# Kernel optimization log

Measured on AMD Instinct MI355X. Metric: run time of the kernel, lower is better.

The kernel has to match this reference:

```python
import jax, jax.numpy as jnp
import numpy as np

TOP_K = 2


def setup_inputs() -> dict:
    key = jax.random.key(0)
    k1, k2, k3, k4, k5 = jax.random.split(key, 5)
    B, S, H, F, E = 4, 2048, 1024, 4096, 8
    scale = 1.0 / np.sqrt(H)
    return {
        "hidden_states": jax.random.normal(k1, (B, S, H), dtype=jnp.float32),
        "gate_w": jax.random.normal(k2, (E, H), dtype=jnp.float32) * scale,
        "w1": jax.random.normal(k3, (E, F, H), dtype=jnp.float32) * scale,
        "w3": jax.random.normal(k4, (E, F, H), dtype=jnp.float32) * scale,
        "w2": jax.random.normal(k5, (E, H, F), dtype=jnp.float32) * (1.0 / np.sqrt(F)),
    }


def reference(hidden_states, gate_w, w1, w3, w2):
    B, S, H = hidden_states.shape
    E = gate_w.shape[0]
    x = hidden_states.reshape(-1, H)                    # [T, H], T = B*S

    router_logits = x @ gate_w.T                        # [T, E]
    probs = jax.nn.softmax(router_logits.astype(jnp.float32), axis=-1)
    top_w, top_i = jax.lax.top_k(probs, TOP_K)          # [T, k]
    top_w = top_w / jnp.sum(top_w, axis=-1, keepdims=True)
    top_w = top_w.astype(x.dtype)

    # combine weight of each expert for each token: [E, T]
    one_hot = jax.nn.one_hot(top_i, E, dtype=x.dtype)   # [T, k, E]
    comb = jnp.einsum("tke,tk->et", one_hot, top_w)

    # loop over experts via scan; tokens not routed to expert e have comb==0,
    # which matches the gather/FFN/scatter-combine of the original exactly.
    def body(acc, wts):
        w1e, w3e, w2e, ce = wts
        h = jax.nn.silu(x @ w1e.T) * (x @ w3e.T)        # [T, F]
        return acc + (h @ w2e.T) * ce[:, None], None

    out0 = jnp.zeros_like(x)
    out, _ = jax.lax.scan(body, out0, (w1, w3, w2, comb))
    return out.reshape(B, S, H), router_logits
```

## Files before the change

kernel.cpp:

```cpp
#include <hip/hip_runtime.h>
#include <hip/hip_bf16.h>

#define T_TOK 8192
#define HDIM  1024
#define FDIM  4096
#define NEXP  8
#define CVT_BLKS 2048

typedef __attribute__((ext_vector_type(8))) short short8;
typedef __attribute__((ext_vector_type(4))) float f32x4;
typedef unsigned short u16;
typedef unsigned int   u32;

#define XB_OFF    0ull
#define W1B_OFF   (XB_OFF   + 16777216ull)
#define W3B_OFF   (W1B_OFF  + 67108864ull)
#define W2B_OFF   (W3B_OFF  + 67108864ull)
#define HBUF_OFF  (W2B_OFF  + 67108864ull)
#define CNT_OFF   (HBUF_OFF + 134217728ull)
#define HOFF_OFF  (CNT_OFF  + 64ull)
#define TLIST_OFF (HOFF_OFF + 64ull)
#define WLIST_OFF (TLIST_OFF + 262144ull)
#define WS_NEED   (WLIST_OFF + 262144ull)

__device__ __forceinline__ u16 f2bf(float f) {
  u32 u = __float_as_uint(f);
  return (u16)((u + 0x7fffu + ((u >> 16) & 1u)) >> 16);
}
__device__ __forceinline__ float bf2f(u16 v) {
  return __uint_as_float((u32)v << 16);
}

__device__ __forceinline__ void gl_lds16(const void* g, void* l) {
  __builtin_amdgcn_global_load_lds(
      (const __attribute__((address_space(1))) void*)g,
      (__attribute__((address_space(3))) void*)l, 16, 0, 0);
}

__global__ __launch_bounds__(256) void prep_kernel(
    const float* __restrict__ x, const float* __restrict__ gw,
    const float* __restrict__ s0, const float* __restrict__ s1,
    u16* __restrict__ d0, u16* __restrict__ d1,
    float* __restrict__ logits, u16* __restrict__ xb,
    int* __restrict__ counts, int* __restrict__ tlist,
    float* __restrict__ wt1, float* __restrict__ wt2,
    int* __restrict__ slot1, int* __restrict__ slot2) {
  if (blockIdx.x < 8192) {
    const int n8 = NEXP * FDIM * HDIM / 8;
    const int total = 2 * n8;
    const int stride = 8192 * 256;
    for (int i = blockIdx.x * 256 + threadIdx.x; i < total; i += stride) {
      int seg = i >> 22;
      int j = i & (n8 - 1);
      const float* s = seg == 0 ? s0 : s1;
      u16* d = seg == 0 ? d0 : d1;
      float4 v0 = ((const float4*)s)[j * 2];
      float4 v1 = ((const float4*)s)[j * 2 + 1];
      uint4 o;
      o.x = (u32)f2bf(v0.x) | ((u32)f2bf(v0.y) << 16);
      o.y = (u32)f2bf(v0.z) | ((u32)f2bf(v0.w) << 16);
      o.z = (u32)f2bf(v1.x) | ((u32)f2bf(v1.y) << 16);
      o.w = (u32)f2bf(v1.z) | ((u32)f2bf(v1.w) << 16);
      ((uint4*)d)[j] = o;
    }
    return;
  }
  const int wid = threadIdx.x >> 6, lane = threadIdx.x & 63;
  const int t = (blockIdx.x - 8192) * 4 + wid;
  const float* xr = x + (size_t)t * HDIM + lane * 16;
  float4 xv[4];
#pragma unroll
  for (int q = 0; q < 4; ++q) xv[q] = ((const float4*)xr)[q];

  u32 pk[8];
#pragma unroll
  for (int q = 0; q < 4; ++q) {
    pk[q * 2 + 0] = (u32)f2bf(xv[q].x) | ((u32)f2bf(xv[q].y) << 16);
    pk[q * 2 + 1] = (u32)f2bf(xv[q].z) | ((u32)f2bf(xv[q].w) << 16);
  }
  u32* xbo = (u32*)(xb + (size_t)t * HDIM + lane * 16);
  ((uint4*)xbo)[0] = make_uint4(pk[0], pk[1], pk[2], pk[3]);
  ((uint4*)xbo)[1] = make_uint4(pk[4], pk[5], pk[6], pk[7]);

  float lg[NEXP];
#pragma unroll
  for (int e = 0; e < NEXP; ++e) {
    const float4* g = (const float4*)(gw + (size_t)e * HDIM + lane * 16);
    float s = 0.f;
#pragma unroll
    for (int q = 0; q < 4; ++q) {
      float4 gv = g[q];
      s += xv[q].x * gv.x + xv[q].y * gv.y + xv[q].z * gv.z + xv[q].w * gv.w;
    }
#pragma unroll
    for (int off = 32; off > 0; off >>= 1) s += __shfl_xor(s, off, 64);
    lg[e] = s;
  }
  if (lane == 0) {
    float* lo = logits + (size_t)t * NEXP;
#pragma unroll
    for (int e = 0; e < NEXP; ++e) lo[e] = lg[e];
    float v1 = -1e30f, v2 = -1e30f; int i1 = 0, i2 = 0;
#pragma unroll
    for (int e = 0; e < NEXP; ++e) {
      float le = lg[e];
      if (le > v1)      { v2 = v1; i2 = i1; v1 = le; i1 = e; }
      else if (le > v2) { v2 = le; i2 = e; }
    }
    float t2 = __expf(v2 - v1);
    float rs = 1.f / (1.f + t2);
    int p1 = atomicAdd(&counts[i1], 1);
    tlist[i1 * T_TOK + p1] = t;
    slot1[t] = (i1 << 16) | p1;  wt1[t] = rs;
    int p2 = atomicAdd(&counts[i2], 1);
    tlist[i2 * T_TOK + p2] = t;
    slot2[t] = (i2 << 16) | p2;  wt2[t] = t2 * rs;
  }
}

__global__ void prefix_kernel(const int* __restrict__ counts, int* __restrict__ hoff) {
  if (threadIdx.x == 0) {
    int s = 0;
    for (int e = 0; e < NEXP; ++e) { hoff[e] = s; s += counts[e]; }
    hoff[NEXP] = s;
  }
}

__global__ __launch_bounds__(256, 4) void ffn1_kernel(
    const u16* __restrict__ xb, const u16* __restrict__ w1b, const u16* __restrict__ w3b,
    u16* __restrict__ hbuf, const int* __restrict__ counts, const int* __restrict__ hoff,
    const int* __restrict__ tlist,
    const float* __restrict__ w2src, u16* __restrict__ w2b) {
  if (blockIdx.x < CVT_BLKS) {
    const int n8 = NEXP * HDIM * FDIM / 8;
    const int stride = CVT_BLKS * 256;
    for (int j = blockIdx.x * 256 + threadIdx.x; j < n8; j += stride) {
      float4 v0 = ((const float4*)w2src)[j * 2];
      float4 v1 = ((const float4*)w2src)[j * 2 + 1];
      uint4 o;
      o.x = (u32)f2bf(v0.x) | ((u32)f2bf(v0.y) << 16);
      o.y = (u32)f2bf(v0.z) | ((u32)f2bf(v0.w) << 16);
      o.z = (u32)f2bf(v1.x) | ((u32)f2bf(v1.y) << 16);
      o.w = (u32)f2bf(v1.z) | ((u32)f2bf(v1.w) << 16);
      ((uint4*)w2b)[j] = o;
    }
    return;
  }
  const int bid = blockIdx.x - CVT_BLKS;
  const int e  = bid & 7;
  const int j  = bid >> 3;
  const int ct = j >> 6;
  const int rt = j & 63;
  const int Ne = counts[e];
  if (rt * 128 >= Ne) return;

  __shared__ u16 LDS[16384];

  const int tid = threadIdx.x;
  const int wid = tid >> 6, lane = tid & 63;
  const int wr = wid >> 1, wc = wid & 1;
  const int lr = lane & 15, lhi = lane >> 4;

  size_t aoff[4];
#pragma unroll
  for (int q = 0; q < 4; ++q) {
    int idx = q * 256 + tid;
    int r = idx >> 3, c = idx & 7;
    int grow = rt * 128 + r;
    int gi = grow < Ne ? grow : Ne - 1;
    aoff[q] = (size_t)tlist[e * T_TOK + gi] * HDIM + (size_t)((c ^ (r & 7)) * 8);
  }
  size_t boff[2];
#pragma unroll
  for (int q = 0; q < 2; ++q) {
    int idx = q * 256 + tid;
    int r = idx >> 3, c = idx & 7;
    boff[q] = ((size_t)e * FDIM + ct * 64 + r) * HDIM + (size_t)((c ^ (r & 7)) * 8);
  }
  const int dW = wid * 64 * 8;

  f32x4 acc1[4][2] = {}, acc3[4][2] = {};

  for (int k0 = 0; k0 < HDIM; k0 += 64) {
    __syncthreads();
#pragma unroll
    for (int q = 0; q < 4; ++q)
      gl_lds16(xb + aoff[q] + k0, LDS + q * 2048 + dW);
#pragma unroll
    for (int q = 0; q < 2; ++q) {
      gl_lds16(w1b + boff[q] + k0, LDS + 8192 + q * 2048 + dW);
      gl_lds16(w3b + boff[q] + k0, LDS + 12288 + q * 2048 + dW);
    }
    __syncthreads();
#pragma unroll
    for (int kk = 0; kk < 2; ++kk) {
      const int chn = ((kk * 4 + lhi) ^ (lr & 7)) * 8;
      short8 af[4], b1f[2], b3f[2];
#pragma unroll
      for (int m = 0; m < 4; ++m)
        af[m] = *(const short8*)(LDS + (wr * 64 + m * 16 + lr) * 64 + chn);
#pragma unroll
      for (int n = 0; n < 2; ++n) {
        int ro = (wc * 32 + n * 16 + lr) * 64 + chn;
        b1f[n] = *(const short8*)(LDS + 8192 + ro);
        b3f[n] = *(const short8*)(LDS + 12288 + ro);
      }
#pragma unroll
      for (int m = 0; m < 4; ++m)
#pragma unroll
        for (int n = 0; n < 2; ++n) {
          acc1[m][n] = __builtin_amdgcn_mfma_f32_16x16x32_bf16(af[m], b1f[n], acc1[m][n], 0, 0, 0);
          acc3[m][n] = __builtin_amdgcn_mfma_f32_16x16x32_bf16(af[m], b3f[n], acc3[m][n], 0, 0, 0);
        }
    }
  }

  const int hb = hoff[e];
  const int rbase = rt * 128 + wr * 64 + lhi * 4;
  const int cbase = ct * 64 + wc * 32 + lr;
#pragma unroll
  for (int m = 0; m < 4; ++m)
#pragma unroll
    for (int i = 0; i < 4; ++i) {
      int grow = rbase + m * 16 + i;
      if (grow < Ne) {
        size_t rowp = (size_t)(hb + grow) * FDIM + cbase;
#pragma unroll
        for (int n = 0; n < 2; ++n) {
          float a1 = acc1[m][n][i], a3 = acc3[m][n][i];
          hbuf[rowp + n * 16] = f2bf((a1 / (1.f + __expf(-a1))) * a3);
        }
      }
    }
}

__global__ __launch_bounds__(256, 4) void ffn2_kernel(
    const u16* __restrict__ hbuf, const u16* __restrict__ w2b,
    u16* __restrict__ ybuf, const int* __restrict__ counts, const int* __restrict__ hoff) {
  const int bid = blockIdx.x;
  const int e  = bid & 7;
  const int j  = bid >> 3;
  const int ct = j >> 6;
  const int rt = j & 63;
  const int Ne = counts[e];
  if (rt * 128 >= Ne) return;
  const int hb = hoff[e];

  __shared__ u16 Alds[128 * 64];
  __shared__ u16 Blds[128 * 64];

  const int tid = threadIdx.x;
  const int wid = tid >> 6, lane = tid & 63;
  const int wr = wid >> 1, wc = wid & 1;
  const int lr = lane & 15, lhi = lane >> 4;

  size_t aoff[4], boff[4]; int ldso[4];
#pragma unroll
  for (int q = 0; q < 4; ++q) {
    int i = wid * 4 + q;
    int r = i * 8 + (lane >> 3);
    int sw = ((lane & 7) ^ (r & 7)) * 8;
    int grow = rt * 128 + r;
    int gi = grow < Ne ? grow : Ne - 1;
    aoff[q] = (size_t)(hb + gi) * FDIM + sw;
    int hr = ct * 128 + r;
    boff[q] = ((size_t)e * HDIM + hr) * FDIM + sw;
    ldso[q] = i * 512;
  }

  f32x4 acc[4][4] = {};

  for (int k0 = 0; k0 < FDIM; k0 += 64) {
    __syncthreads();
#pragma unroll
    for (int q = 0; q < 4; ++q) {
      gl_lds16(hbuf + aoff[q] + k0, Alds + ldso[q]);
      gl_lds16(w2b + boff[q] + k0, Blds + ldso[q]);
    }
    __syncthreads();
#pragma unroll
    for (int kk = 0; kk < 2; ++kk) {
      const int swo = ((kk * 4 + lhi) ^ (lr & 7)) * 8;
      short8 af[4], bf_[4];
#pragma unroll
      for (int m = 0; m < 4; ++m)
        af[m] = *(const short8*)(Alds + (wr * 64 + m * 16 + lr) * 64 + swo);
#pragma unroll
      for (int n = 0; n < 4; ++n)
        bf_[n] = *(const short8*)(Blds + (wc * 64 + n * 16 + lr) * 64 + swo);
#pragma unroll
      for (int m = 0; m < 4; ++m)
#pragma unroll
        for (int n = 0; n < 4; ++n)
          acc[m][n] = __builtin_amdgcn_mfma_f32_16x16x32_bf16(af[m], bf_[n], acc[m][n], 0, 0, 0);
    }
  }

  const int rb = rt * 128 + wr * 64 + lhi * 4;
  const int cb = ct * 128 + wc * 64 + lr;
#pragma unroll
  for (int m = 0; m < 4; ++m)
#pragma unroll
    for (int i = 0; i < 4; ++i) {
      int grow = rb + m * 16 + i;
      if (grow < Ne) {
        u16* yp = ybuf + (size_t)(hb + grow) * HDIM + cb;
#pragma unroll
        for (int n = 0; n < 4; ++n)
          yp[n * 16] = f2bf(acc[m][n][i]);
      }
    }
}

__global__ __launch_bounds__(256) void combine_kernel(
    const u16* __restrict__ ybuf, const int* __restrict__ slot1, const int* __restrict__ slot2,
    const float* __restrict__ wt1, const float* __restrict__ wt2,
    const int* __restrict__ hoff, float* __restrict__ out) {
  int idx = blockIdx.x * 256 + threadIdx.x;
  int t = idx >> 7, c8 = (idx & 127) * 8;
  int s1 = slot1[t], s2 = slot2[t];
  float w1 = wt1[t], w2 = wt2[t];
  size_t r1 = (size_t)(hoff[s1 >> 16] + (s1 & 0xFFFF)) * HDIM + c8;
  size_t r2 = (size_t)(hoff[s2 >> 16] + (s2 & 0xFFFF)) * HDIM + c8;
  short8 y1 = *(const short8*)(ybuf + r1);
  short8 y2 = *(const short8*)(ybuf + r2);
  float* op = out + (size_t)t * HDIM + c8;
#pragma unroll
  for (int k = 0; k < 8; ++k)
    op[k] = w1 * bf2f((u16)y1[k]) + w2 * bf2f((u16)y2[k]);
}

extern "C" void kernel_launch(void* const* d_in, const int* in_sizes, int n_in,
                              void* d_out, int out_size, void* d_ws, size_t ws_size,
                              hipStream_t stream) {
  (void)in_sizes; (void)n_in; (void)out_size;
  if (ws_size < WS_NEED) return;

  const float* x  = (const float*)d_in[0];
  const float* gw = (const float*)d_in[1];
  const float* w1 = (const float*)d_in[2];
  const float* w3 = (const float*)d_in[3];
  const float* w2 = (const float*)d_in[4];
  float* out = (float*)d_out;
  float* logits = out + (size_t)T_TOK * HDIM;

  char* ws = (char*)d_ws;
  u16* xb    = (u16*)(ws + XB_OFF);
  u16* w1b   = (u16*)(ws + W1B_OFF);
  u16* w3b   = (u16*)(ws + W3B_OFF);
  u16* w2b   = (u16*)(ws + W2B_OFF);
  u16* hbuf  = (u16*)(ws + HBUF_OFF);
  u16* ybuf  = (u16*)(ws + W1B_OFF);
  int* counts = (int*)(ws + CNT_OFF);
  int* hoffp  = (int*)(ws + HOFF_OFF);
  int* tlist  = (int*)(ws + TLIST_OFF);
  float* wt1  = (float*)(ws + WLIST_OFF);
  float* wt2  = wt1 + T_TOK;
  int* slot1  = (int*)(wt2 + T_TOK);
  int* slot2  = slot1 + T_TOK;

  hipMemsetAsync(counts, 0, NEXP * sizeof(int), stream);

  prep_kernel<<<8192 + 2048, 256, 0, stream>>>(x, gw, w1, w3, w1b, w3b,
                                               logits, xb, counts, tlist,
                                               wt1, wt2, slot1, slot2);
  prefix_kernel<<<1, 64, 0, stream>>>(counts, hoffp);
  ffn1_kernel<<<CVT_BLKS + NEXP * 64 * 64, 256, 0, stream>>>(
      xb, w1b, w3b, hbuf, counts, hoffp, tlist, w2, w2b);
  ffn2_kernel<<<NEXP * 64 * 8, 256, 0, stream>>>(hbuf, w2b, ybuf, counts, hoffp);
  combine_kernel<<<T_TOK * 128 / 256, 256, 0, stream>>>(ybuf, slot1, slot2, wt1, wt2, hoffp, out);
}
```

Baseline: 780.8 us.

## Switch expert GEMMs to 32x32x16 MFMA and inline prefix offsets

Both expert FFN GEMM kernels now use 32x32x16 bf16 MFMA tiles instead of 16x16x32. This halves the number of LDS fragment reads per MFMA and cuts instruction count, with the epilogue rewritten for the 32x32 accumulator layout. The separate single-thread prefix kernel is removed: each block computes its expert row offset from counts directly, which saves a tiny launch at the cost of a few redundant loads per block. The larger accumulator vectors may raise register pressure under the 4-blocks launch bound.

```diff
diff --git a/kernel.cpp b/kernel.cpp
--- a/kernel.cpp
+++ b/kernel.cpp
@@ -7,8 +7,8 @@
 #define NEXP  8
 #define CVT_BLKS 2048
 
-typedef __attribute__((ext_vector_type(8))) short short8;
-typedef __attribute__((ext_vector_type(4))) float f32x4;
+typedef __attribute__((ext_vector_type(8)))  short short8;
+typedef __attribute__((ext_vector_type(16))) float f32x16;
 typedef unsigned short u16;
 typedef unsigned int   u32;
 
@@ -18,8 +18,7 @@
 #define W2B_OFF   (W3B_OFF  + 67108864ull)
 #define HBUF_OFF  (W2B_OFF  + 67108864ull)
 #define CNT_OFF   (HBUF_OFF + 134217728ull)
-#define HOFF_OFF  (CNT_OFF  + 64ull)
-#define TLIST_OFF (HOFF_OFF + 64ull)
+#define TLIST_OFF (CNT_OFF  + 128ull)
 #define WLIST_OFF (TLIST_OFF + 262144ull)
 #define WS_NEED   (WLIST_OFF + 262144ull)
 
@@ -118,18 +117,9 @@
   }
 }
 
-__global__ void prefix_kernel(const int* __restrict__ counts, int* __restrict__ hoff) {
-  if (threadIdx.x == 0) {
-    int s = 0;
-    for (int e = 0; e < NEXP; ++e) { hoff[e] = s; s += counts[e]; }
-    hoff[NEXP] = s;
-  }
-}
-
 __global__ __launch_bounds__(256, 4) void ffn1_kernel(
     const u16* __restrict__ xb, const u16* __restrict__ w1b, const u16* __restrict__ w3b,
-    u16* __restrict__ hbuf, const int* __restrict__ counts, const int* __restrict__ hoff,
-    const int* __restrict__ tlist,
+    u16* __restrict__ hbuf, const int* __restrict__ counts, const int* __restrict__ tlist,
     const float* __restrict__ w2src, u16* __restrict__ w2b) {
   if (blockIdx.x < CVT_BLKS) {
     const int n8 = NEXP * HDIM * FDIM / 8;
@@ -153,13 +143,16 @@
   const int rt = j & 63;
   const int Ne = counts[e];
   if (rt * 128 >= Ne) return;
+  int hb = 0;
+#pragma unroll
+  for (int i = 0; i < NEXP; ++i) hb += (i < e) ? counts[i] : 0;
 
   __shared__ u16 LDS[16384];
 
   const int tid = threadIdx.x;
   const int wid = tid >> 6, lane = tid & 63;
   const int wr = wid >> 1, wc = wid & 1;
-  const int lr = lane & 15, lhi = lane >> 4;
+  const int l31 = lane & 31, l5 = lane >> 5;
 
   size_t aoff[4];
 #pragma unroll
@@ -177,9 +170,11 @@
     int r = idx >> 3, c = idx & 7;
     boff[q] = ((size_t)e * FDIM + ct * 64 + r) * HDIM + (size_t)((c ^ (r & 7)) * 8);
   }
-  const int dW = wid * 64 * 8;
-
-  f32x4 acc1[4][2] = {}, acc3[4][2] = {};
+  const int dW = wid * 512;
+
+  const int rowA0 = wr * 64 + l31;
+  const int rowB  = wc * 32 + l31;
+  f32x16 acc1[2] = {{0}}, acc3[2] = {{0}};
 
   for (int k0 = 0; k0 < HDIM; k0 += 64) {
     __syncthreads();
@@ -193,50 +188,41 @@
     }
     __syncthreads();
 #pragma unroll
-    for (int kk = 0; kk < 2; ++kk) {
-      const int chn = ((kk * 4 + lhi) ^ (lr & 7)) * 8;
-      short8 af[4], b1f[2], b3f[2];
-#pragma unroll
-      for (int m = 0; m < 4; ++m)
-        af[m] = *(const short8*)(LDS + (wr * 64 + m * 16 + lr) * 64 + chn);
-#pragma unroll
-      for (int n = 0; n < 2; ++n) {
-        int ro = (wc * 32 + n * 16 + lr) * 64 + chn;
-        b1f[n] = *(const short8*)(LDS + 8192 + ro);
-        b3f[n] = *(const short8*)(LDS + 12288 + ro);
-      }
-#pragma unroll
-      for (int m = 0; m < 4; ++m)
-#pragma unroll
-        for (int n = 0; n < 2; ++n) {
-          acc1[m][n] = __builtin_amdgcn_mfma_f32_16x16x32_bf16(af[m], b1f[n], acc1[m][n], 0, 0, 0);
-          acc3[m][n] = __builtin_amdgcn_mfma_f32_16x16x32_bf16(af[m], b3f[n], acc3[m][n], 0, 0, 0);
-        }
-    }
-  }
-
-  const int hb = hoff[e];
-  const int rbase = rt * 128 + wr * 64 + lhi * 4;
-  const int cbase = ct * 64 + wc * 32 + lr;
-#pragma unroll
-  for (int m = 0; m < 4; ++m)
-#pragma unroll
-    for (int i = 0; i < 4; ++i) {
-      int grow = rbase + m * 16 + i;
+    for (int kk = 0; kk < 4; ++kk) {
+      const int cbase = kk * 2 + l5;
+      short8 af[2], b1v, b3v;
+#pragma unroll
+      for (int m = 0; m < 2; ++m) {
+        int r = rowA0 + m * 32;
+        af[m] = *(const short8*)(LDS + r * 64 + ((cbase ^ (r & 7)) * 8));
+      }
+      b1v = *(const short8*)(LDS + 8192  + rowB * 64 + ((cbase ^ (rowB & 7)) * 8));
+      b3v = *(const short8*)(LDS + 12288 + rowB * 64 + ((cbase ^ (rowB & 7)) * 8));
+#pragma unroll
+      for (int m = 0; m < 2; ++m) {
+        acc1[m] = __builtin_amdgcn_mfma_f32_32x32x16_bf16(af[m], b1v, acc1[m], 0, 0, 0);
+        acc3[m] = __builtin_amdgcn_mfma_f32_32x32x16_bf16(af[m], b3v, acc3[m], 0, 0, 0);
+      }
+    }
+  }
+
+  const int rbase = rt * 128 + wr * 64;
+  const int cbase = ct * 64 + wc * 32 + l31;
+#pragma unroll
+  for (int m = 0; m < 2; ++m)
+#pragma unroll
+    for (int r16 = 0; r16 < 16; ++r16) {
+      int grow = rbase + m * 32 + (r16 & 3) + 8 * (r16 >> 2) + 4 * l5;
       if (grow < Ne) {
-        size_t rowp = (size_t)(hb + grow) * FDIM + cbase;
-#pragma unroll
-        for (int n = 0; n < 2; ++n) {
-          float a1 = acc1[m][n][i], a3 = acc3[m][n][i];
-          hbuf[rowp + n * 16] = f2bf((a1 / (1.f + __expf(-a1))) * a3);
-        }
+        float a1 = acc1[m][r16], a3 = acc3[m][r16];
+        hbuf[(size_t)(hb + grow) * FDIM + cbase] = f2bf((a1 / (1.f + __expf(-a1))) * a3);
       }
     }
 }
 
 __global__ __launch_bounds__(256, 4) void ffn2_kernel(
     const u16* __restrict__ hbuf, const u16* __restrict__ w2b,
-    u16* __restrict__ ybuf, const int* __restrict__ counts, const int* __restrict__ hoff) {
+    u16* __restrict__ ybuf, const int* __restrict__ counts) {
   const int bid = blockIdx.x;
   const int e  = bid & 7;
   const int j  = bid >> 3;
@@ -244,7 +230,9 @@
   const int rt = j & 63;
   const int Ne = counts[e];
   if (rt * 128 >= Ne) return;
-  const int hb = hoff[e];
+  int hb = 0;
+#pragma unroll
+  for (int i = 0; i < NEXP; ++i) hb += (i < e) ? counts[i] : 0;
 
   __shared__ u16 Alds[128 * 64];
   __shared__ u16 Blds[128 * 64];
@@ -252,7 +240,7 @@
   const int tid = threadIdx.x;
   const int wid = tid >> 6, lane = tid & 63;
   const int wr = wid >> 1, wc = wid & 1;
-  const int lr = lane & 15, lhi = lane >> 4;
+  const int l31 = lane & 31, l5 = lane >> 5;
 
   size_t aoff[4], boff[4]; int ldso[4];
 #pragma unroll
@@ -268,7 +256,9 @@
     ldso[q] = i * 512;
   }
 
-  f32x4 acc[4][4] = {};
+  const int rowA0 = wr * 64 + l31;
+  const int rowB0 = wc * 64 + l31;
+  f32x16 acc[2][2] = {{{0}}};
 
   for (int k0 = 0; k0 < FDIM; k0 += 64) {
     __syncthreads();
@@ -279,35 +269,39 @@
     }
     __syncthreads();
 #pragma unroll
-    for (int kk = 0; kk < 2; ++kk) {
-      const int swo = ((kk * 4 + lhi) ^ (lr & 7)) * 8;
-      short8 af[4], bf_[4];
-#pragma unroll
-      for (int m = 0; m < 4; ++m)
-        af[m] = *(const short8*)(Alds + (wr * 64 + m * 16 + lr) * 64 + swo);
-#pragma unroll
-      for (int n = 0; n < 4; ++n)
-        bf_[n] = *(const short8*)(Blds + (wc * 64 + n * 16 + lr) * 64 + swo);
-#pragma unroll
-      for (int m = 0; m < 4; ++m)
-#pragma unroll
-        for (int n = 0; n < 4; ++n)
-          acc[m][n] = __builtin_amdgcn_mfma_f32_16x16x32_bf16(af[m], bf_[n], acc[m][n], 0, 0, 0);
-    }
-  }
-
-  const int rb = rt * 128 + wr * 64 + lhi * 4;
-  const int cb = ct * 128 + wc * 64 + lr;
-#pragma unroll
-  for (int m = 0; m < 4; ++m)
-#pragma unroll
-    for (int i = 0; i < 4; ++i) {
-      int grow = rb + m * 16 + i;
+    for (int kk = 0; kk < 4; ++kk) {
+      const int cbase = kk * 2 + l5;
+      short8 af[2], bf_[2];
+#pragma unroll
+      for (int m = 0; m < 2; ++m) {
+        int r = rowA0 + m * 32;
+        af[m] = *(const short8*)(Alds + r * 64 + ((cbase ^ (r & 7)) * 8));
+      }
+#pragma unroll
+      for (int n = 0; n < 2; ++n) {
+        int r = rowB0 + n * 32;
+        bf_[n] = *(const short8*)(Blds + r * 64 + ((cbase ^ (r & 7)) * 8));
+      }
+#pragma unroll
+      for (int m = 0; m < 2; ++m)
+#pragma unroll
+        for (int n = 0; n < 2; ++n)
+          acc[m][n] = __builtin_amdgcn_mfma_f32_32x32x16_bf16(af[m], bf_[n], acc[m][n], 0, 0, 0);
+    }
+  }
+
+  const int rbase = rt * 128 + wr * 64;
+  const int cb0 = ct * 128 + wc * 64 + l31;
+#pragma unroll
+  for (int m = 0; m < 2; ++m)
+#pragma unroll
+    for (int r16 = 0; r16 < 16; ++r16) {
+      int grow = rbase + m * 32 + (r16 & 3) + 8 * (r16 >> 2) + 4 * l5;
       if (grow < Ne) {
-        u16* yp = ybuf + (size_t)(hb + grow) * HDIM + cb;
-#pragma unroll
-        for (int n = 0; n < 4; ++n)
-          yp[n * 16] = f2bf(acc[m][n][i]);
+        u16* yp = ybuf + (size_t)(hb + grow) * HDIM + cb0;
+#pragma unroll
+        for (int n = 0; n < 2; ++n)
+          yp[n * 32] = f2bf(acc[m][n][r16]);
       }
     }
 }
@@ -315,13 +309,17 @@
 __global__ __launch_bounds__(256) void combine_kernel(
     const u16* __restrict__ ybuf, const int* __restrict__ slot1, const int* __restrict__ slot2,
     const float* __restrict__ wt1, const float* __restrict__ wt2,
-    const int* __restrict__ hoff, float* __restrict__ out) {
+    const int* __restrict__ counts, float* __restrict__ out) {
+  int pre[NEXP + 1];
+  pre[0] = 0;
+#pragma unroll
+  for (int i = 0; i < NEXP; ++i) pre[i + 1] = pre[i] + counts[i];
   int idx = blockIdx.x * 256 + threadIdx.x;
   int t = idx >> 7, c8 = (idx & 127) * 8;
   int s1 = slot1[t], s2 = slot2[t];
   float w1 = wt1[t], w2 = wt2[t];
-  size_t r1 = (size_t)(hoff[s1 >> 16] + (s1 & 0xFFFF)) * HDIM + c8;
-  size_t r2 = (size_t)(hoff[s2 >> 16] + (s2 & 0xFFFF)) * HDIM + c8;
+  size_t r1 = (size_t)(pre[s1 >> 16] + (s1 & 0xFFFF)) * HDIM + c8;
+  size_t r2 = (size_t)(pre[s2 >> 16] + (s2 & 0xFFFF)) * HDIM + c8;
   short8 y1 = *(const short8*)(ybuf + r1);
   short8 y2 = *(const short8*)(ybuf + r2);
   float* op = out + (size_t)t * HDIM + c8;
@@ -352,7 +350,6 @@
   u16* hbuf  = (u16*)(ws + HBUF_OFF);
   u16* ybuf  = (u16*)(ws + W1B_OFF);
   int* counts = (int*)(ws + CNT_OFF);
-  int* hoffp  = (int*)(ws + HOFF_OFF);
   int* tlist  = (int*)(ws + TLIST_OFF);
   float* wt1  = (float*)(ws + WLIST_OFF);
   float* wt2  = wt1 + T_TOK;
@@ -364,9 +361,8 @@
   prep_kernel<<<8192 + 2048, 256, 0, stream>>>(x, gw, w1, w3, w1b, w3b,
                                                logits, xb, counts, tlist,
                                                wt1, wt2, slot1, slot2);
-  prefix_kernel<<<1, 64, 0, stream>>>(counts, hoffp);
   ffn1_kernel<<<CVT_BLKS + NEXP * 64 * 64, 256, 0, stream>>>(
-      xb, w1b, w3b, hbuf, counts, hoffp, tlist, w2, w2b);
-  ffn2_kernel<<<NEXP * 64 * 8, 256, 0, stream>>>(hbuf, w2b, ybuf, counts, hoffp);
-  combine_kernel<<<T_TOK * 128 / 256, 256, 0, stream>>>(ybuf, slot1, slot2, wt1, wt2, hoffp, out);
-}
+      xb, w1b, w3b, hbuf, counts, tlist, w2, w2b);
+  ffn2_kernel<<<NEXP * 64 * 8, 256, 0, stream>>>(hbuf, w2b, ybuf, counts);
+  combine_kernel<<<T_TOK * 128 / 256, 256, 0, stream>>>(ybuf, slot1, slot2, wt1, wt2, counts, out);
+}
```

New measurement: 829.4 us. 6.2% more time.

## Restructure FFN1 into 512-thread blocks splitting w1/w3 across wave sets; drop prefix kernel

Applied to the files above, without the earlier changes.

The gate/up GEMM kernel now uses 512-thread blocks covering 128 F-columns. Four waves compute the w1 product and four compute the w3 product, sharing the same A tile in LDS, and the w3 results are passed through LDS in bf16 for the SiLU-multiply epilogue. This is meant to raise A-tile reuse and halve the number of blocks. The separate prefix-sum kernel is removed and each kernel recomputes expert offsets from the counts, saving one launch. The w3 partial product is now rounded to bf16 before the multiply, which slightly changes precision, and the extra LDS round-trip and syncs add cost.

```diff
diff --git a/kernel.cpp b/kernel.cpp
--- a/kernel.cpp
+++ b/kernel.cpp
@@ -5,7 +5,7 @@
 #define HDIM  1024
 #define FDIM  4096
 #define NEXP  8
-#define CVT_BLKS 2048
+#define CVT_BLKS 1024
 
 typedef __attribute__((ext_vector_type(8))) short short8;
 typedef __attribute__((ext_vector_type(4))) float f32x4;
@@ -18,8 +18,7 @@
 #define W2B_OFF   (W3B_OFF  + 67108864ull)
 #define HBUF_OFF  (W2B_OFF  + 67108864ull)
 #define CNT_OFF   (HBUF_OFF + 134217728ull)
-#define HOFF_OFF  (CNT_OFF  + 64ull)
-#define TLIST_OFF (HOFF_OFF + 64ull)
+#define TLIST_OFF (CNT_OFF  + 128ull)
 #define WLIST_OFF (TLIST_OFF + 262144ull)
 #define WS_NEED   (WLIST_OFF + 262144ull)
 
@@ -118,23 +117,14 @@
   }
 }
 
-__global__ void prefix_kernel(const int* __restrict__ counts, int* __restrict__ hoff) {
-  if (threadIdx.x == 0) {
-    int s = 0;
-    for (int e = 0; e < NEXP; ++e) { hoff[e] = s; s += counts[e]; }
-    hoff[NEXP] = s;
-  }
-}
-
-__global__ __launch_bounds__(256, 4) void ffn1_kernel(
+__global__ __launch_bounds__(512, 4) void ffn1_kernel(
     const u16* __restrict__ xb, const u16* __restrict__ w1b, const u16* __restrict__ w3b,
-    u16* __restrict__ hbuf, const int* __restrict__ counts, const int* __restrict__ hoff,
-    const int* __restrict__ tlist,
+    u16* __restrict__ hbuf, const int* __restrict__ counts, const int* __restrict__ tlist,
     const float* __restrict__ w2src, u16* __restrict__ w2b) {
   if (blockIdx.x < CVT_BLKS) {
     const int n8 = NEXP * HDIM * FDIM / 8;
-    const int stride = CVT_BLKS * 256;
-    for (int j = blockIdx.x * 256 + threadIdx.x; j < n8; j += stride) {
+    const int stride = CVT_BLKS * 512;
+    for (int j = blockIdx.x * 512 + threadIdx.x; j < n8; j += stride) {
       float4 v0 = ((const float4*)w2src)[j * 2];
       float4 v1 = ((const float4*)w2src)[j * 2 + 1];
       uint4 o;
@@ -153,18 +143,23 @@
   const int rt = j & 63;
   const int Ne = counts[e];
   if (rt * 128 >= Ne) return;
-
-  __shared__ u16 LDS[16384];
+  int hb = 0;
+#pragma unroll
+  for (int i = 0; i < NEXP; ++i) hb += (i < e) ? counts[i] : 0;
+
+  __shared__ u16 LDS[24576];
 
   const int tid = threadIdx.x;
   const int wid = tid >> 6, lane = tid & 63;
-  const int wr = wid >> 1, wc = wid & 1;
+  const int tset = wid >> 2;
+  const int patch = wid & 3;
+  const int wr = patch >> 1, wc = patch & 1;
   const int lr = lane & 15, lhi = lane >> 4;
 
-  size_t aoff[4];
-#pragma unroll
-  for (int q = 0; q < 4; ++q) {
-    int idx = q * 256 + tid;
+  size_t aoff[2];
+#pragma unroll
+  for (int q = 0; q < 2; ++q) {
+    int idx = q * 512 + tid;
     int r = idx >> 3, c = idx & 7;
     int grow = rt * 128 + r;
     int gi = grow < Ne ? grow : Ne - 1;
@@ -173,70 +168,77 @@
   size_t boff[2];
 #pragma unroll
   for (int q = 0; q < 2; ++q) {
-    int idx = q * 256 + tid;
+    int idx = q * 512 + tid;
     int r = idx >> 3, c = idx & 7;
-    boff[q] = ((size_t)e * FDIM + ct * 64 + r) * HDIM + (size_t)((c ^ (r & 7)) * 8);
-  }
-  const int dW = wid * 64 * 8;
-
-  f32x4 acc1[4][2] = {}, acc3[4][2] = {};
+    boff[q] = ((size_t)e * FDIM + ct * 128 + r) * HDIM + (size_t)((c ^ (r & 7)) * 8);
+  }
+  const int dW = wid * 512;
+
+  f32x4 acc[4][4] = {};
+  const int bbase = 8192 + tset * 8192;
 
   for (int k0 = 0; k0 < HDIM; k0 += 64) {
     __syncthreads();
 #pragma unroll
-    for (int q = 0; q < 4; ++q)
-      gl_lds16(xb + aoff[q] + k0, LDS + q * 2048 + dW);
-#pragma unroll
     for (int q = 0; q < 2; ++q) {
-      gl_lds16(w1b + boff[q] + k0, LDS + 8192 + q * 2048 + dW);
-      gl_lds16(w3b + boff[q] + k0, LDS + 12288 + q * 2048 + dW);
+      gl_lds16(xb  + aoff[q] + k0, LDS + q * 4096 + dW);
+      gl_lds16(w1b + boff[q] + k0, LDS + 8192 + q * 4096 + dW);
+      gl_lds16(w3b + boff[q] + k0, LDS + 16384 + q * 4096 + dW);
     }
     __syncthreads();
 #pragma unroll
     for (int kk = 0; kk < 2; ++kk) {
       const int chn = ((kk * 4 + lhi) ^ (lr & 7)) * 8;
-      short8 af[4], b1f[2], b3f[2];
+      short8 af[4], bf_[4];
 #pragma unroll
       for (int m = 0; m < 4; ++m)
         af[m] = *(const short8*)(LDS + (wr * 64 + m * 16 + lr) * 64 + chn);
 #pragma unroll
-      for (int n = 0; n < 2; ++n) {
-        int ro = (wc * 32 + n * 16 + lr) * 64 + chn;
-        b1f[n] = *(const short8*)(LDS + 8192 + ro);
-        b3f[n] = *(const short8*)(LDS + 12288 + ro);
-      }
+      for (int n = 0; n < 4; ++n)
+        bf_[n] = *(const short8*)(LDS + bbase + (wc * 64 + n * 16 + lr) * 64 + chn);
 #pragma unroll
       for (int m = 0; m < 4; ++m)
 #pragma unroll
-        for (int n = 0; n < 2; ++n) {
-          acc1[m][n] = __builtin_amdgcn_mfma_f32_16x16x32_bf16(af[m], b1f[n], acc1[m][n], 0, 0, 0);
-          acc3[m][n] = __builtin_amdgcn_mfma_f32_16x16x32_bf16(af[m], b3f[n], acc3[m][n], 0, 0, 0);
-        }
-    }
-  }
-
-  const int hb = hoff[e];
-  const int rbase = rt * 128 + wr * 64 + lhi * 4;
-  const int cbase = ct * 64 + wc * 32 + lr;
-#pragma unroll
-  for (int m = 0; m < 4; ++m)
-#pragma unroll
-    for (int i = 0; i < 4; ++i) {
-      int grow = rbase + m * 16 + i;
-      if (grow < Ne) {
-        size_t rowp = (size_t)(hb + grow) * FDIM + cbase;
-#pragma unroll
-        for (int n = 0; n < 2; ++n) {
-          float a1 = acc1[m][n][i], a3 = acc3[m][n][i];
-          hbuf[rowp + n * 16] = f2bf((a1 / (1.f + __expf(-a1))) * a3);
+        for (int n = 0; n < 4; ++n)
+          acc[m][n] = __builtin_amdgcn_mfma_f32_16x16x32_bf16(af[m], bf_[n], acc[m][n], 0, 0, 0);
+    }
+  }
+
+  __syncthreads();
+  if (tset == 1) {
+#pragma unroll
+    for (int m = 0; m < 4; ++m)
+#pragma unroll
+      for (int n = 0; n < 4; ++n)
+#pragma unroll
+        for (int i = 0; i < 4; ++i)
+          LDS[patch * 4096 + (m * 16 + lhi * 4 + i) * 64 + n * 16 + lr] = f2bf(acc[m][n][i]);
+  }
+  __syncthreads();
+  if (tset == 0) {
+    const int rbase = rt * 128 + wr * 64 + lhi * 4;
+    const int cbase = ct * 128 + wc * 64 + lr;
+#pragma unroll
+    for (int m = 0; m < 4; ++m)
+#pragma unroll
+      for (int i = 0; i < 4; ++i) {
+        int grow = rbase + m * 16 + i;
+        if (grow < Ne) {
+          size_t rowp = (size_t)(hb + grow) * FDIM + cbase;
+#pragma unroll
+          for (int n = 0; n < 4; ++n) {
+            float a1 = acc[m][n][i];
+            float a3 = bf2f(LDS[patch * 4096 + (m * 16 + lhi * 4 + i) * 64 + n * 16 + lr]);
+            hbuf[rowp + n * 16] = f2bf((a1 / (1.f + __expf(-a1))) * a3);
+          }
         }
       }
-    }
+  }
 }
 
 __global__ __launch_bounds__(256, 4) void ffn2_kernel(
     const u16* __restrict__ hbuf, const u16* __restrict__ w2b,
-    u16* __restrict__ ybuf, const int* __restrict__ counts, const int* __restrict__ hoff) {
+    u16* __restrict__ ybuf, const int* __restrict__ counts) {
   const int bid = blockIdx.x;
   const int e  = bid & 7;
   const int j  = bid >> 3;
@@ -244,7 +246,9 @@
   const int rt = j & 63;
   const int Ne = counts[e];
   if (rt * 128 >= Ne) return;
-  const int hb = hoff[e];
+  int hb = 0;
+#pragma unroll
+  for (int i = 0; i < NEXP; ++i) hb += (i < e) ? counts[i] : 0;
 
   __shared__ u16 Alds[128 * 64];
   __shared__ u16 Blds[128 * 64];
@@ -315,13 +319,17 @@
 __global__ __launch_bounds__(256) void combine_kernel(
     const u16* __restrict__ ybuf, const int* __restrict__ slot1, const int* __restrict__ slot2,
     const float* __restrict__ wt1, const float* __restrict__ wt2,
-    const int* __restrict__ hoff, float* __restrict__ out) {
+    const int* __restrict__ counts, float* __restrict__ out) {
+  int pre[NEXP + 1];
+  pre[0] = 0;
+#pragma unroll
+  for (int i = 0; i < NEXP; ++i) pre[i + 1] = pre[i] + counts[i];
   int idx = blockIdx.x * 256 + threadIdx.x;
   int t = idx >> 7, c8 = (idx & 127) * 8;
   int s1 = slot1[t], s2 = slot2[t];
   float w1 = wt1[t], w2 = wt2[t];
-  size_t r1 = (size_t)(hoff[s1 >> 16] + (s1 & 0xFFFF)) * HDIM + c8;
-  size_t r2 = (size_t)(hoff[s2 >> 16] + (s2 & 0xFFFF)) * HDIM + c8;
+  size_t r1 = (size_t)(pre[s1 >> 16] + (s1 & 0xFFFF)) * HDIM + c8;
+  size_t r2 = (size_t)(pre[s2 >> 16] + (s2 & 0xFFFF)) * HDIM + c8;
   short8 y1 = *(const short8*)(ybuf + r1);
   short8 y2 = *(const short8*)(ybuf + r2);
   float* op = out + (size_t)t * HDIM + c8;
@@ -352,7 +360,6 @@
   u16* hbuf  = (u16*)(ws + HBUF_OFF);
   u16* ybuf  = (u16*)(ws + W1B_OFF);
   int* counts = (int*)(ws + CNT_OFF);
-  int* hoffp  = (int*)(ws + HOFF_OFF);
   int* tlist  = (int*)(ws + TLIST_OFF);
   float* wt1  = (float*)(ws + WLIST_OFF);
   float* wt2  = wt1 + T_TOK;
@@ -364,9 +371,8 @@
   prep_kernel<<<8192 + 2048, 256, 0, stream>>>(x, gw, w1, w3, w1b, w3b,
                                                logits, xb, counts, tlist,
                                                wt1, wt2, slot1, slot2);
-  prefix_kernel<<<1, 64, 0, stream>>>(counts, hoffp);
-  ffn1_kernel<<<CVT_BLKS + NEXP * 64 * 64, 256, 0, stream>>>(
-      xb, w1b, w3b, hbuf, counts, hoffp, tlist, w2, w2b);
-  ffn2_kernel<<<NEXP * 64 * 8, 256, 0, stream>>>(hbuf, w2b, ybuf, counts, hoffp);
-  combine_kernel<<<T_TOK * 128 / 256, 256, 0, stream>>>(ybuf, slot1, slot2, wt1, wt2, hoffp, out);
-}
+  ffn1_kernel<<<CVT_BLKS + NEXP * 64 * 32, 512, 0, stream>>>(
+      xb, w1b, w3b, hbuf, counts, tlist, w2, w2b);
+  ffn2_kernel<<<NEXP * 64 * 8, 256, 0, stream>>>(hbuf, w2b, ybuf, counts);
+  combine_kernel<<<T_TOK * 128 / 256, 256, 0, stream>>>(ybuf, slot1, slot2, wt1, wt2, counts, out);
+}
```

New measurement: 844.6 us. 1.08x slower.
